# Optimization experiments

Hardware: AMD Instinct MI355X
Metric: run time of the kernel (lower is better)

## Reference

```python
import jax, jax.numpy as jnp
import numpy as np

N_ENTITIES = 100000
EMBED = 64
BATCH = 4096
TEMPERATURE = 0.2


def _infonce(v1, v2, temperature):
    # v1, v2: [B, d]
    B = v1.shape[0]
    sim11 = v1 @ v1.T  # [B,B]
    sim22 = v2 @ v2.T
    sim12 = v1 @ v2.T
    eye = jnp.eye(B, dtype=bool)
    neg_inf = jnp.float32(-jnp.inf)
    sim11 = jnp.where(eye, neg_inf, sim11)
    sim22 = jnp.where(eye, neg_inf, sim22)
    logits1 = jnp.concatenate([sim12, sim11], axis=-1)          # [B,2B]
    logits2 = jnp.concatenate([sim22, sim12.T], axis=-1)        # [B,2B]
    logits = jnp.concatenate([logits1, logits2], axis=0) / temperature  # [2B,2B]
    targets = jnp.arange(2 * B)
    logp = jax.nn.log_softmax(logits, axis=-1)
    return -jnp.mean(jnp.take_along_axis(logp, targets[:, None], axis=-1))


def setup_inputs() -> dict:
    key = jax.random.key(0)
    k1, k2, k3, k4, k5, k6 = jax.random.split(key, 6)
    return {
        "input_u_list": jax.random.randint(k1, (BATCH,), 0, N_ENTITIES),
        "input_i_list": jax.random.randint(k2, (BATCH,), 0, N_ENTITIES),
        "u_sub1_embeddings": jax.random.normal(k3, (N_ENTITIES, EMBED), dtype=jnp.float32),
        "i_sub1_embeddings": jax.random.normal(k4, (N_ENTITIES, EMBED), dtype=jnp.float32),
        "u_sub2_embeddings": jax.random.normal(k5, (N_ENTITIES, EMBED), dtype=jnp.float32),
        "i_sub2_embeddings": jax.random.normal(k6, (N_ENTITIES, EMBED), dtype=jnp.float32),
    }


def reference(input_u_list, input_i_list, u_sub1_embeddings, i_sub1_embeddings,
              u_sub2_embeddings, i_sub2_embeddings):
    # user branch: gather + L2-normalize
    u1 = u_sub1_embeddings[input_u_list]
    u2 = u_sub2_embeddings[input_u_list]
    u1 = u1 / jnp.linalg.norm(u1, axis=1, keepdims=True)
    u2 = u2 / jnp.linalg.norm(u2, axis=1, keepdims=True)
    user_cl_loss = _infonce(u1, u2, TEMPERATURE)
    # item branch: gather only (the original does NOT normalize items)
    i1 = i_sub1_embeddings[input_i_list]
    i2 = i_sub2_embeddings[input_i_list]
    item_cl_loss = _infonce(i1, i2, TEMPERATURE)
    return user_cl_loss + item_cl_loss
```

## Files before the change

kernel.cpp:

```cpp
#include <hip/hip_runtime.h>
#include <hip/hip_bf16.h>
#include <math.h>

#define B_SZ   4096
#define D      64
#define RPB    8192
#define NCHUNK 8
#define TPC    8
#define NPART  16
#define LN2    0.69314718055994531f
#define PRESCALE 2.6857914f

typedef __attribute__((ext_vector_type(8))) short  bf16x8;
typedef __attribute__((ext_vector_type(4))) float  f32x4;

__device__ __forceinline__ float fexp2(float x) { return __builtin_amdgcn_exp2f(x); }

typedef const __attribute__((address_space(1))) unsigned int* gptr_t;
typedef __attribute__((address_space(3))) unsigned int* lptr_t;
__device__ __forceinline__ void stage16(const void* g, void* l) {
    __builtin_amdgcn_global_load_lds((gptr_t)g, (lptr_t)l, 16, 0, 0);
}


__global__ __launch_bounds__(256) void gather_kernel(
    const int* __restrict__ u_idx, const int* __restrict__ i_idx,
    const float* __restrict__ u1e, const float* __restrict__ i1e,
    const float* __restrict__ u2e, const float* __restrict__ i2e,
    __hip_bfloat16* __restrict__ Xbf, float* __restrict__ dots)
{
    const int tid  = threadIdx.x;
    const int wave = tid >> 6, lane = tid & 63;
    const int g      = blockIdx.x * 4 + wave;
    const int branch = g >> 12;
    const int i      = g & (B_SZ - 1);
    const int idx    = (branch == 0) ? u_idx[i] : i_idx[i];
    const float* s1  = (branch == 0) ? u1e : i1e;
    const float* s2  = (branch == 0) ? u2e : i2e;

    float v1 = s1[(size_t)idx * D + lane];
    float v2 = s2[(size_t)idx * D + lane];
    if (branch == 0) {
        float a = v1 * v1, b = v2 * v2;
        #pragma unroll
        for (int o = 32; o > 0; o >>= 1) {
            a += __shfl_xor(a, o, 64);
            b += __shfl_xor(b, o, 64);
        }
        v1 *= rsqrtf(a);
        v2 *= rsqrtf(b);
    }
    float p = v1 * v2;
    #pragma unroll
    for (int o = 32; o > 0; o >>= 1) p += __shfl_xor(p, o, 64);
    if (lane == 0) dots[g] = p;

    const size_t row1 = (size_t)branch * RPB + i;
    Xbf[row1 * D + lane]          = __float2bfloat16(v1 * PRESCALE);
    Xbf[(row1 + B_SZ) * D + lane] = __float2bfloat16(v2 * PRESCALE);
}

template<int IS_USER>
__device__ __forceinline__ void gram_body(
    const __hip_bfloat16* __restrict__ Xb, float2* __restrict__ P,
    const int bx, char* sm)
{
    const int tid   = threadIdx.x;
    const int chunk = blockIdx.y;
    const int r0    = bx * 128;

    const int wave = tid >> 6, lane = tid & 63;
    const int wm = wave >> 1, wn = wave & 1;
    const int quad = lane >> 4, tx = lane & 15;

    const int srow_b = wave * 32 + (lane >> 3);
    const int scb    = ((lane & 7) * 16) ^ ((lane >> 3) << 4);
    const char* Xbytes = (const char*)Xb;

    {
        const char* src = Xbytes + (size_t)(chunk * TPC) * 16384;
        #pragma unroll
        for (int k = 0; k < 4; ++k)
            stage16(src + (srow_b + k * 8) * 128 + scb,
                    sm + wave * 4096 + k * 1024);
    }

    bf16x8 afr[4][2];
    const __hip_bfloat16* Ap = Xb + (size_t)(r0 + wm * 64 + tx) * D + quad * 8;
    #pragma unroll
    for (int mt = 0; mt < 4; ++mt)
        #pragma unroll
        for (int ks = 0; ks < 2; ++ks)
            afr[mt][ks] = *(const bf16x8*)(Ap + mt * 16 * D + ks * 32);

    float m_run[16], s_run[16];
    #pragma unroll
    for (int r = 0; r < 16; ++r) { m_run[r] = -INFINITY; s_run[r] = 0.f; }

    const int lrq  = wm * 64 + quad * 4;
    const int lcol = wn * 64 + tx;

    const int rbase = (wn * 64 + tx) * 128;
    const int key   = (tx & 7) << 4;
    const int cb0   = (quad * 16) ^ key;
    const int cb1   = (64 + quad * 16) ^ key;

    __syncthreads();

    #pragma unroll 1
    for (int t = 0; t < TPC; ++t) {
        const int ct  = chunk * TPC + t;
        const int cur = (t & 1) << 14;

        if (t + 1 < TPC) {
            const char* src = Xbytes + (size_t)(ct + 1) * 16384;
            char* dst = sm + (((t + 1) & 1) << 14) + wave * 4096;
            #pragma unroll
            for (int k = 0; k < 4; ++k)
                stage16(src + (srow_b + k * 8) * 128 + scb, dst + k * 1024);
        }

        bf16x8 b0[4], b1[4];
        #pragma unroll
        for (int nt = 0; nt < 4; ++nt) {
            b0[nt] = *(const bf16x8*)(sm + cur + rbase + nt * 2048 + cb0);
            b1[nt] = *(const bf16x8*)(sm + cur + rbase + nt * 2048 + cb1);
        }

        f32x4 acc[4][4];
        const f32x4 z = {0.f, 0.f, 0.f, 0.f};
        #pragma unroll
        for (int nt = 0; nt < 4; ++nt)
            #pragma unroll
            for (int mt = 0; mt < 4; ++mt)
                acc[mt][nt] = __builtin_amdgcn_mfma_f32_16x16x32_bf16(afr[mt][0], b0[nt], z, 0, 0, 0);
        #pragma unroll
        for (int nt = 0; nt < 4; ++nt)
            #pragma unroll
            for (int mt = 0; mt < 4; ++mt)
                acc[mt][nt] = __builtin_amdgcn_mfma_f32_16x16x32_bf16(afr[mt][1], b1[nt], acc[mt][nt], 0, 0, 0);

        const bool diag = (ct == bx);
        #pragma unroll
        for (int mt = 0; mt < 4; ++mt) {
            #pragma unroll
            for (int rr = 0; rr < 4; ++rr) {
                float y0 = acc[mt][0][rr], y1 = acc[mt][1][rr],
                      y2 = acc[mt][2][rr], y3 = acc[mt][3][rr];
                if (diag) {
                    const int dr = lrq + mt * 16 + rr - lcol;
                    if (dr == 0)  y0 = -INFINITY;
                    if (dr == 16) y1 = -INFINITY;
                    if (dr == 32) y2 = -INFINITY;
                    if (dr == 48) y3 = -INFINITY;
                }
                const int r = mt * 4 + rr;
                if (IS_USER) {
                    s_run[r] += fexp2(y0) + fexp2(y1) + fexp2(y2) + fexp2(y3);
                } else {
                    float mx   = fmaxf(fmaxf(y0, y1), fmaxf(y2, y3));
                    float newm = fmaxf(m_run[r], mx);
                    s_run[r] = s_run[r] * fexp2(m_run[r] - newm)
                             + fexp2(y0 - newm) + fexp2(y1 - newm)
                             + fexp2(y2 - newm) + fexp2(y3 - newm);
                    m_run[r] = newm;
                }
            }
        }

        __syncthreads();
    }

    #pragma unroll
    for (int r = 0; r < 16; ++r) {
        float m = IS_USER ? 0.f : m_run[r];
        float s = s_run[r];
        #pragma unroll
        for (int o = 1; o < 16; o <<= 1) {
            if (IS_USER) {
                s += __shfl_xor(s, o, 64);
            } else {
                float om = __shfl_xor(m, o, 64);
                float os = __shfl_xor(s, o, 64);
                float M  = fmaxf(m, om);
                s = s * fexp2(m - M) + os * fexp2(om - M);
                m = M;
            }
        }
        if (tx == 0) {
            const int grow = r0 + wm * 64 + (r >> 2) * 16 + quad * 4 + (r & 3);
            P[(size_t)grow * NPART + chunk * 2 + wn] = make_float2(m, s);
        }
    }
}

__global__ __launch_bounds__(256, 3) void gram_lse_fused(
    const __hip_bfloat16* __restrict__ Xb0, float2* __restrict__ P0)
{
    __shared__ __align__(16) char sm[32768];
    const int branch = blockIdx.x & 1;
    const int bx     = blockIdx.x >> 1;
    const __hip_bfloat16* Xb = Xb0 + (size_t)branch * RPB * D;
    float2* P = P0 + (size_t)branch * RPB * NPART;
    if (branch == 0) gram_body<1>(Xb, P, bx, sm);
    else             gram_body<0>(Xb, P, bx, sm);
}

__global__ __launch_bounds__(256) void merge_kernel(
    const float2* __restrict__ P, const float* __restrict__ dots,
    float* __restrict__ out)
{
    __shared__ float red[4];
    const int tid  = threadIdx.x;
    const int wave = tid >> 6, lane = tid & 63;

    float vsum = 0.f;
    #pragma unroll
    for (int k = 0; k < 8; ++k) {
        const int vb  = blockIdx.x * 8 + k;
        const int gw  = vb * 4 + wave;
        const int row = gw * 4 + (lane >> 4);
        const int c   = lane & 15;

        float2 p = P[(size_t)row * NPART + c];
        float m = p.x, s = p.y;
        #pragma unroll
        for (int o = 1; o < 16; o <<= 1) {
            float om = __shfl_xor(m, o, 64);
            float os = __shfl_xor(s, o, 64);
            float M  = fmaxf(m, om);
            s = s * fexp2(m - M) + os * fexp2(om - M);
            m = M;
        }

        if ((lane & 15) == 0)
            vsum += LN2 * (m + log2f(s)) * (1.0f / (float)RPB);
        if (tid < 8)
            vsum -= dots[vb * 8 + tid] * (5.0f / (float)B_SZ);
    }

    float v = vsum;
    #pragma unroll
    for (int o = 32; o > 0; o >>= 1) v += __shfl_xor(v, o, 64);
    if (lane == 0) red[wave] = v;
    __syncthreads();
    if (tid == 0)
        atomicAdd(out, red[0] + red[1] + red[2] + red[3]);
}

extern "C" void kernel_launch(void* const* d_in, const int* in_sizes, int n_in,
                              void* d_out, int out_size, void* d_ws, size_t ws_size,
                              hipStream_t stream) {
    const int*   u_idx = (const int*)d_in[0];
    const int*   i_idx = (const int*)d_in[1];
    const float* u1e   = (const float*)d_in[2];
    const float* i1e   = (const float*)d_in[3];
    const float* u2e   = (const float*)d_in[4];
    const float* i2e   = (const float*)d_in[5];
    float* out = (float*)d_out;

    __hip_bfloat16* Xbf = (__hip_bfloat16*)d_ws;
    float*  dots = (float*)((char*)d_ws + 2 * RPB * D * 2);
    float2* P    = (float2*)((char*)dots + RPB * sizeof(float));

    hipMemsetAsync(out, 0, sizeof(float), stream);

    gather_kernel<<<dim3(2048), dim3(256), 0, stream>>>(
        u_idx, i_idx, u1e, i1e, u2e, i2e, Xbf, dots);
    gram_lse_fused<<<dim3(128, NCHUNK), dim3(256), 0, stream>>>(Xbf, P);
    merge_kernel<<<dim3(128), dim3(256), 0, stream>>>(P, dots, out);
}
```

Before: 169.2 us.

## Halve gram grid with two chunks per block, lazy max rescale, fold memset

The gram kernel now launches 512 blocks instead of 1024, and each block handles two column chunks in one continuous 16-tile double-buffered loop. This amortizes the A-fragment load and prologue and lets prefetch run across the chunk boundary, but halves the number of blocks available to fill the GPU. The item-branch online softmax only rescales when the tile max exceeds the running max by more than a threshold, which removes most exp2 rescale work per tile. The output zeroing moves from hipMemsetAsync into the gather kernel to drop one API call.

```diff
diff --git a/kernel.cpp b/kernel.cpp
--- a/kernel.cpp
+++ b/kernel.cpp
@@ -10,6 +10,7 @@
 #define NPART  16
 #define LN2    0.69314718055994531f
 #define PRESCALE 2.6857914f
+#define DEFER_THR 60.0f
 
 typedef __attribute__((ext_vector_type(8))) short  bf16x8;
 typedef __attribute__((ext_vector_type(4))) float  f32x4;
@@ -27,9 +28,11 @@
     const int* __restrict__ u_idx, const int* __restrict__ i_idx,
     const float* __restrict__ u1e, const float* __restrict__ i1e,
     const float* __restrict__ u2e, const float* __restrict__ i2e,
-    __hip_bfloat16* __restrict__ Xbf, float* __restrict__ dots)
+    __hip_bfloat16* __restrict__ Xbf, float* __restrict__ dots,
+    float* __restrict__ out)
 {
     const int tid  = threadIdx.x;
+    if (blockIdx.x == 0 && tid == 0) *out = 0.f;
     const int wave = tid >> 6, lane = tid & 63;
     const int g      = blockIdx.x * 4 + wave;
     const int branch = g >> 12;
@@ -63,12 +66,10 @@
 template<int IS_USER>
 __device__ __forceinline__ void gram_body(
     const __hip_bfloat16* __restrict__ Xb, float2* __restrict__ P,
-    const int bx, char* sm)
-{
-    const int tid   = threadIdx.x;
-    const int chunk = blockIdx.y;
-    const int r0    = bx * 128;
-
+    const int bx, const int cp, char* sm)
+{
+    const int tid  = threadIdx.x;
+    const int r0   = bx * 128;
     const int wave = tid >> 6, lane = tid & 63;
     const int wm = wave >> 1, wn = wave & 1;
     const int quad = lane >> 4, tx = lane & 15;
@@ -78,7 +79,7 @@
     const char* Xbytes = (const char*)Xb;
 
     {
-        const char* src = Xbytes + (size_t)(chunk * TPC) * 16384;
+        const char* src = Xbytes + (size_t)(cp * TPC) * 16384;
         #pragma unroll
         for (int k = 0; k < 4; ++k)
             stage16(src + (srow_b + k * 8) * 128 + scb,
@@ -108,13 +109,17 @@
     __syncthreads();
 
     #pragma unroll 1
-    for (int t = 0; t < TPC; ++t) {
-        const int ct  = chunk * TPC + t;
-        const int cur = (t & 1) << 14;
-
-        if (t + 1 < TPC) {
-            const char* src = Xbytes + (size_t)(ct + 1) * 16384;
-            char* dst = sm + (((t + 1) & 1) << 14) + wave * 4096;
+    for (int g = 0; g < 16; ++g) {
+        const int t     = g & 7;
+        const int chunk = cp + (g >> 3) * 4;
+        const int ct    = chunk * TPC + t;
+        const int cur   = (g & 1) << 14;
+
+        if (g + 1 < 16) {
+            const int gn  = g + 1;
+            const int ctn = (cp + (gn >> 3) * 4) * TPC + (gn & 7);
+            const char* src = Xbytes + (size_t)ctn * 16384;
+            char* dst = sm + ((gn & 1) << 14) + wave * 4096;
             #pragma unroll
             for (int k = 0; k < 4; ++k)
                 stage16(src + (srow_b + k * 8) * 128 + scb, dst + k * 1024);
@@ -158,39 +163,45 @@
                 if (IS_USER) {
                     s_run[r] += fexp2(y0) + fexp2(y1) + fexp2(y2) + fexp2(y3);
                 } else {
-                    float mx   = fmaxf(fmaxf(y0, y1), fmaxf(y2, y3));
-                    float newm = fmaxf(m_run[r], mx);
-                    s_run[r] = s_run[r] * fexp2(m_run[r] - newm)
-                             + fexp2(y0 - newm) + fexp2(y1 - newm)
-                             + fexp2(y2 - newm) + fexp2(y3 - newm);
-                    m_run[r] = newm;
+                    float mx = fmaxf(fmaxf(y0, y1), fmaxf(y2, y3));
+                    if (__builtin_expect(mx > m_run[r] + DEFER_THR, 0)) {
+                        s_run[r] *= fexp2(m_run[r] - mx);
+                        m_run[r] = mx;
+                    }
+                    const float m = m_run[r];
+                    s_run[r] += fexp2(y0 - m) + fexp2(y1 - m)
+                              + fexp2(y2 - m) + fexp2(y3 - m);
                 }
             }
         }
 
+        if (t == 7) {
+            #pragma unroll
+            for (int r = 0; r < 16; ++r) {
+                float m = IS_USER ? 0.f : m_run[r];
+                float s = s_run[r];
+                #pragma unroll
+                for (int o = 1; o < 16; o <<= 1) {
+                    if (IS_USER) {
+                        s += __shfl_xor(s, o, 64);
+                    } else {
+                        float om = __shfl_xor(m, o, 64);
+                        float os = __shfl_xor(s, o, 64);
+                        float M  = fmaxf(m, om);
+                        s = s * fexp2(m - M) + os * fexp2(om - M);
+                        m = M;
+                    }
+                }
+                if (tx == 0) {
+                    const int grow = r0 + wm * 64 + (r >> 2) * 16 + quad * 4 + (r & 3);
+                    P[(size_t)grow * NPART + chunk * 2 + wn] = make_float2(m, s);
+                }
+                m_run[r] = -INFINITY;
+                s_run[r] = 0.f;
+            }
+        }
+
         __syncthreads();
-    }
-
-    #pragma unroll
-    for (int r = 0; r < 16; ++r) {
-        float m = IS_USER ? 0.f : m_run[r];
-        float s = s_run[r];
-        #pragma unroll
-        for (int o = 1; o < 16; o <<= 1) {
-            if (IS_USER) {
-                s += __shfl_xor(s, o, 64);
-            } else {
-                float om = __shfl_xor(m, o, 64);
-                float os = __shfl_xor(s, o, 64);
-                float M  = fmaxf(m, om);
-                s = s * fexp2(m - M) + os * fexp2(om - M);
-                m = M;
-            }
-        }
-        if (tx == 0) {
-            const int grow = r0 + wm * 64 + (r >> 2) * 16 + quad * 4 + (r & 3);
-            P[(size_t)grow * NPART + chunk * 2 + wn] = make_float2(m, s);
-        }
     }
 }
 
@@ -198,12 +209,14 @@
     const __hip_bfloat16* __restrict__ Xb0, float2* __restrict__ P0)
 {
     __shared__ __align__(16) char sm[32768];
-    const int branch = blockIdx.x & 1;
-    const int bx     = blockIdx.x >> 1;
+    const int bid    = blockIdx.x;
+    const int branch = bid & 1;
+    const int bx     = (bid >> 1) & 63;
+    const int cp     = bid >> 7;
     const __hip_bfloat16* Xb = Xb0 + (size_t)branch * RPB * D;
     float2* P = P0 + (size_t)branch * RPB * NPART;
-    if (branch == 0) gram_body<1>(Xb, P, bx, sm);
-    else             gram_body<0>(Xb, P, bx, sm);
+    if (branch == 0) gram_body<1>(Xb, P, bx, cp, sm);
+    else             gram_body<0>(Xb, P, bx, cp, sm);
 }
 
 __global__ __launch_bounds__(256) void merge_kernel(
@@ -263,10 +276,8 @@
     float*  dots = (float*)((char*)d_ws + 2 * RPB * D * 2);
     float2* P    = (float2*)((char*)dots + RPB * sizeof(float));
 
-    hipMemsetAsync(out, 0, sizeof(float), stream);
-
     gather_kernel<<<dim3(2048), dim3(256), 0, stream>>>(
-        u_idx, i_idx, u1e, i1e, u2e, i2e, Xbf, dots);
-    gram_lse_fused<<<dim3(128, NCHUNK), dim3(256), 0, stream>>>(Xbf, P);
+        u_idx, i_idx, u1e, i1e, u2e, i2e, Xbf, dots, out);
+    gram_lse_fused<<<dim3(512), dim3(256), 0, stream>>>(Xbf, P);
     merge_kernel<<<dim3(128), dim3(256), 0, stream>>>(P, dots, out);
 }
```

Result: slower. 179.6 us (+6.1%).

## Use deferred-max online softmax, interleave MFMA with epilogue, fold output zeroing

Applied to the files above, without the earlier changes.

The item-branch online log-sum-exp now starts its running max at zero and only rescales when a logit exceeds the current max by a threshold, so most elements need one exp and no max/rescale work. The MFMA loop is restructured per column tile, so each tile's accumulators are consumed right away and fewer registers are live, and launch bounds drop to 2 waves per SIMD. The output memset is folded into the gather kernel to remove a separate launch. Risks: the threshold scheme relies on the exp2 range to avoid overflow, and lower occupancy may reduce latency hiding.

```diff
diff --git a/kernel.cpp b/kernel.cpp
--- a/kernel.cpp
+++ b/kernel.cpp
@@ -10,6 +10,7 @@
 #define NPART  16
 #define LN2    0.69314718055994531f
 #define PRESCALE 2.6857914f
+#define DEFER_THR 60.0f
 
 typedef __attribute__((ext_vector_type(8))) short  bf16x8;
 typedef __attribute__((ext_vector_type(4))) float  f32x4;
@@ -27,9 +28,11 @@
     const int* __restrict__ u_idx, const int* __restrict__ i_idx,
     const float* __restrict__ u1e, const float* __restrict__ i1e,
     const float* __restrict__ u2e, const float* __restrict__ i2e,
-    __hip_bfloat16* __restrict__ Xbf, float* __restrict__ dots)
+    __hip_bfloat16* __restrict__ Xbf, float* __restrict__ dots,
+    float* __restrict__ out)
 {
     const int tid  = threadIdx.x;
+    if (blockIdx.x == 0 && tid == 0) *out = 0.f;
     const int wave = tid >> 6, lane = tid & 63;
     const int g      = blockIdx.x * 4 + wave;
     const int branch = g >> 12;
@@ -68,7 +71,6 @@
     const int tid   = threadIdx.x;
     const int chunk = blockIdx.y;
     const int r0    = bx * 128;
-
     const int wave = tid >> 6, lane = tid & 63;
     const int wm = wave >> 1, wn = wave & 1;
     const int quad = lane >> 4, tx = lane & 15;
@@ -95,7 +97,7 @@
 
     float m_run[16], s_run[16];
     #pragma unroll
-    for (int r = 0; r < 16; ++r) { m_run[r] = -INFINITY; s_run[r] = 0.f; }
+    for (int r = 0; r < 16; ++r) { m_run[r] = 0.f; s_run[r] = 0.f; }
 
     const int lrq  = wm * 64 + quad * 4;
     const int lcol = wn * 64 + tx;
@@ -120,50 +122,38 @@
                 stage16(src + (srow_b + k * 8) * 128 + scb, dst + k * 1024);
         }
 
-        bf16x8 b0[4], b1[4];
+        const bool diag = (ct == bx);
+        const f32x4 z = {0.f, 0.f, 0.f, 0.f};
+
         #pragma unroll
         for (int nt = 0; nt < 4; ++nt) {
-            b0[nt] = *(const bf16x8*)(sm + cur + rbase + nt * 2048 + cb0);
-            b1[nt] = *(const bf16x8*)(sm + cur + rbase + nt * 2048 + cb1);
-        }
-
-        f32x4 acc[4][4];
-        const f32x4 z = {0.f, 0.f, 0.f, 0.f};
-        #pragma unroll
-        for (int nt = 0; nt < 4; ++nt)
+            const bf16x8 b0 = *(const bf16x8*)(sm + cur + rbase + nt * 2048 + cb0);
+            const bf16x8 b1 = *(const bf16x8*)(sm + cur + rbase + nt * 2048 + cb1);
+            f32x4 acc[4];
             #pragma unroll
             for (int mt = 0; mt < 4; ++mt)
-                acc[mt][nt] = __builtin_amdgcn_mfma_f32_16x16x32_bf16(afr[mt][0], b0[nt], z, 0, 0, 0);
-        #pragma unroll
-        for (int nt = 0; nt < 4; ++nt)
+                acc[mt] = __builtin_amdgcn_mfma_f32_16x16x32_bf16(afr[mt][0], b0, z, 0, 0, 0);
             #pragma unroll
             for (int mt = 0; mt < 4; ++mt)
-                acc[mt][nt] = __builtin_amdgcn_mfma_f32_16x16x32_bf16(afr[mt][1], b1[nt], acc[mt][nt], 0, 0, 0);
-
-        const bool diag = (ct == bx);
-        #pragma unroll
-        for (int mt = 0; mt < 4; ++mt) {
-            #pragma unroll
-            for (int rr = 0; rr < 4; ++rr) {
-                float y0 = acc[mt][0][rr], y1 = acc[mt][1][rr],
-                      y2 = acc[mt][2][rr], y3 = acc[mt][3][rr];
-                if (diag) {
-                    const int dr = lrq + mt * 16 + rr - lcol;
-                    if (dr == 0)  y0 = -INFINITY;
-                    if (dr == 16) y1 = -INFINITY;
-                    if (dr == 32) y2 = -INFINITY;
-                    if (dr == 48) y3 = -INFINITY;
-                }
-                const int r = mt * 4 + rr;
-                if (IS_USER) {
-                    s_run[r] += fexp2(y0) + fexp2(y1) + fexp2(y2) + fexp2(y3);
-                } else {
-                    float mx   = fmaxf(fmaxf(y0, y1), fmaxf(y2, y3));
-                    float newm = fmaxf(m_run[r], mx);
-                    s_run[r] = s_run[r] * fexp2(m_run[r] - newm)
-                             + fexp2(y0 - newm) + fexp2(y1 - newm)
-                             + fexp2(y2 - newm) + fexp2(y3 - newm);
-                    m_run[r] = newm;
+                acc[mt] = __builtin_amdgcn_mfma_f32_16x16x32_bf16(afr[mt][1], b1, acc[mt], 0, 0, 0);
+
+            #pragma unroll
+            for (int mt = 0; mt < 4; ++mt) {
+                #pragma unroll
+                for (int rr = 0; rr < 4; ++rr) {
+                    float y = acc[mt][rr];
+                    if (diag && (lrq + mt * 16 + rr - lcol == nt * 16))
+                        y = -INFINITY;
+                    const int r = mt * 4 + rr;
+                    if (IS_USER) {
+                        s_run[r] += fexp2(y);
+                    } else {
+                        if (__builtin_expect(y > m_run[r] + DEFER_THR, 0)) {
+                            s_run[r] *= fexp2(m_run[r] - y);
+                            m_run[r] = y;
+                        }
+                        s_run[r] += fexp2(y - m_run[r]);
+                    }
                 }
             }
         }
@@ -194,7 +184,7 @@
     }
 }
 
-__global__ __launch_bounds__(256, 3) void gram_lse_fused(
+__global__ __launch_bounds__(256, 2) void gram_lse_fused(
     const __hip_bfloat16* __restrict__ Xb0, float2* __restrict__ P0)
 {
     __shared__ __align__(16) char sm[32768];
@@ -263,10 +253,8 @@
     float*  dots = (float*)((char*)d_ws + 2 * RPB * D * 2);
     float2* P    = (float2*)((char*)dots + RPB * sizeof(float));
 
-    hipMemsetAsync(out, 0, sizeof(float), stream);
-
     gather_kernel<<<dim3(2048), dim3(256), 0, stream>>>(
-        u_idx, i_idx, u1e, i1e, u2e, i2e, Xbf, dots);
+        u_idx, i_idx, u1e, i1e, u2e, i2e, Xbf, dots, out);
     gram_lse_fused<<<dim3(128, NCHUNK), dim3(256), 0, stream>>>(Xbf, P);
     merge_kernel<<<dim3(128), dim3(256), 0, stream>>>(P, dots, out);
 }
```

New measurement: 202.3 us. 19.5% more time.

## Split gram blocks into 128-thread column halves and fold output zeroing into gather

Applied to the files above, without the earlier changes.

The gram/LSE kernel now runs 2048 blocks of 128 threads. Each block owns one half of the column tile (wn) and stages only that half into a 16KB LDS double buffer, where before 1024 blocks of 256 threads each held 32KB. The aim is more resident blocks and better load balance across the CUs. The separate hipMemsetAsync on the output is removed, and the first gather thread writes zero instead, saving one API call. The cost is that every block loads its own A fragments, so A reads double, and the zero write must land before merge's atomics, which stream ordering guarantees.

```diff
diff --git a/kernel.cpp b/kernel.cpp
--- a/kernel.cpp
+++ b/kernel.cpp
@@ -27,9 +27,11 @@
     const int* __restrict__ u_idx, const int* __restrict__ i_idx,
     const float* __restrict__ u1e, const float* __restrict__ i1e,
     const float* __restrict__ u2e, const float* __restrict__ i2e,
-    __hip_bfloat16* __restrict__ Xbf, float* __restrict__ dots)
+    __hip_bfloat16* __restrict__ Xbf, float* __restrict__ dots,
+    float* __restrict__ out)
 {
     const int tid  = threadIdx.x;
+    if (blockIdx.x == 0 && tid == 0) *out = 0.f;
     const int wave = tid >> 6, lane = tid & 63;
     const int g      = blockIdx.x * 4 + wave;
     const int branch = g >> 12;
@@ -63,26 +65,24 @@
 template<int IS_USER>
 __device__ __forceinline__ void gram_body(
     const __hip_bfloat16* __restrict__ Xb, float2* __restrict__ P,
-    const int bx, char* sm)
-{
-    const int tid   = threadIdx.x;
-    const int chunk = blockIdx.y;
-    const int r0    = bx * 128;
-
-    const int wave = tid >> 6, lane = tid & 63;
-    const int wm = wave >> 1, wn = wave & 1;
+    const int bx, const int chunk, const int wn, char* sm)
+{
+    const int tid  = threadIdx.x;
+    const int r0   = bx * 128;
+    const int wm   = tid >> 6;
+    const int lane = tid & 63;
     const int quad = lane >> 4, tx = lane & 15;
 
-    const int srow_b = wave * 32 + (lane >> 3);
+    const int srow_b = wm * 8 + (lane >> 3);
     const int scb    = ((lane & 7) * 16) ^ ((lane >> 3) << 4);
     const char* Xbytes = (const char*)Xb;
 
     {
-        const char* src = Xbytes + (size_t)(chunk * TPC) * 16384;
+        const char* src = Xbytes + ((size_t)(chunk * TPC) * 128 + wn * 64) * 128;
         #pragma unroll
         for (int k = 0; k < 4; ++k)
-            stage16(src + (srow_b + k * 8) * 128 + scb,
-                    sm + wave * 4096 + k * 1024);
+            stage16(src + (srow_b + k * 16) * 128 + scb,
+                    sm + k * 2048 + wm * 1024);
     }
 
     bf16x8 afr[4][2];
@@ -100,7 +100,7 @@
     const int lrq  = wm * 64 + quad * 4;
     const int lcol = wn * 64 + tx;
 
-    const int rbase = (wn * 64 + tx) * 128;
+    const int rbase = tx * 128;
     const int key   = (tx & 7) << 4;
     const int cb0   = (quad * 16) ^ key;
     const int cb1   = (64 + quad * 16) ^ key;
@@ -110,14 +110,14 @@
     #pragma unroll 1
     for (int t = 0; t < TPC; ++t) {
         const int ct  = chunk * TPC + t;
-        const int cur = (t & 1) << 14;
+        const int cur = (t & 1) << 13;
 
         if (t + 1 < TPC) {
-            const char* src = Xbytes + (size_t)(ct + 1) * 16384;
-            char* dst = sm + (((t + 1) & 1) << 14) + wave * 4096;
+            const char* src = Xbytes + ((size_t)(ct + 1) * 128 + wn * 64) * 128;
+            char* dst = sm + (((t + 1) & 1) << 13) + wm * 1024;
             #pragma unroll
             for (int k = 0; k < 4; ++k)
-                stage16(src + (srow_b + k * 8) * 128 + scb, dst + k * 1024);
+                stage16(src + (srow_b + k * 16) * 128 + scb, dst + k * 2048);
         }
 
         bf16x8 b0[4], b1[4];
@@ -194,16 +194,19 @@
     }
 }
 
-__global__ __launch_bounds__(256, 3) void gram_lse_fused(
+__global__ __launch_bounds__(128, 3) void gram_lse_fused(
     const __hip_bfloat16* __restrict__ Xb0, float2* __restrict__ P0)
 {
-    __shared__ __align__(16) char sm[32768];
-    const int branch = blockIdx.x & 1;
-    const int bx     = blockIdx.x >> 1;
+    __shared__ __align__(16) char sm[16384];
+    const int bid    = blockIdx.x;
+    const int branch = bid & 1;
+    const int wn     = (bid >> 1) & 1;
+    const int bx     = (bid >> 2) & 63;
+    const int chunk  = bid >> 8;
     const __hip_bfloat16* Xb = Xb0 + (size_t)branch * RPB * D;
     float2* P = P0 + (size_t)branch * RPB * NPART;
-    if (branch == 0) gram_body<1>(Xb, P, bx, sm);
-    else             gram_body<0>(Xb, P, bx, sm);
+    if (branch == 0) gram_body<1>(Xb, P, bx, chunk, wn, sm);
+    else             gram_body<0>(Xb, P, bx, chunk, wn, sm);
 }
 
 __global__ __launch_bounds__(256) void merge_kernel(
@@ -263,10 +266,8 @@
     float*  dots = (float*)((char*)d_ws + 2 * RPB * D * 2);
     float2* P    = (float2*)((char*)dots + RPB * sizeof(float));
 
-    hipMemsetAsync(out, 0, sizeof(float), stream);
-
     gather_kernel<<<dim3(2048), dim3(256), 0, stream>>>(
-        u_idx, i_idx, u1e, i1e, u2e, i2e, Xbf, dots);
-    gram_lse_fused<<<dim3(128, NCHUNK), dim3(256), 0, stream>>>(Xbf, P);
+        u_idx, i_idx, u1e, i1e, u2e, i2e, Xbf, dots, out);
+    gram_lse_fused<<<dim3(2048), dim3(128), 0, stream>>>(Xbf, P);
     merge_kernel<<<dim3(128), dim3(256), 0, stream>>>(P, dots, out);
 }
```

Result: slower. 176.4 us (+4.3%).
